# Optimization experiments

Measured on AMD Instinct MI355X. Metric: run time of the kernel, lower is better.

Reference implementation:

```python
import jax, jax.numpy as jnp
import numpy as np
from jax import lax

# dims
B, H, W, C = 32, 64, 64, 256
FEATURES, HEADS, NQ = 256, 8, 2
K, STRIDE, PAD = 3, 2, 1
HD = FEATURES // HEADS  # head dim = 32


def setup_inputs() -> dict:
    key = jax.random.key(0)
    ks = jax.random.split(key, 7)
    x = jax.random.normal(ks[0], (B, H, W, C), jnp.float32)
    # learned shared queries: truncated normal * sqrt(1/head_dim)
    query = jax.random.truncated_normal(ks[1], -2.0, 2.0, (NQ, FEATURES), jnp.float32) * np.float32(np.sqrt(1.0 / HD))
    Wk = jax.random.normal(ks[2], (C, FEATURES), jnp.float32) * np.float32(np.sqrt(1.0 / C))  # lecun
    Wv = jax.random.normal(ks[3], (C, FEATURES), jnp.float32) * np.float32(np.sqrt(1.0 / C))
    rpe_bias = jax.random.truncated_normal(ks[4], -2.0, 2.0, (K * K, NQ * HEADS), jnp.float32) * np.float32(0.02)
    attn_scale_w = jax.random.normal(ks[5], (K * K, NQ * HEADS), jnp.float32) * np.float32(0.02)
    Wo = jax.random.normal(ks[6], (FEATURES, FEATURES), jnp.float32) * np.float32(np.sqrt(1.0 / FEATURES))
    return {"x": x, "query": query, "Wk": Wk, "Wv": Wv,
            "rpe_bias": rpe_bias, "attn_scale_w": attn_scale_w, "Wo": Wo}


def _qna_forward(x, query, Wk, Wv, rpe_bias, attn_scale_w, Wo):
    # --- queries: reshape to [NQ, HEADS, HD], unit-normalize per head, depth-scale ---
    q = query.reshape(NQ, HEADS, HD)
    q = q / (jnp.linalg.norm(q, axis=-1, keepdims=True) + 1e-6)
    q = q / jnp.sqrt(HD).astype(q.dtype)

    # --- fused QK: (q Wk^T) applied to x, never materializing per-window keys ---
    Wk_r = Wk.reshape(C, HEADS, HD)
    qWk = jnp.einsum('qHd,DHd->DqH', q, Wk_r)              # [C, NQ, HEADS]
    cost = jnp.einsum('bijD,DqH->bijqH', x, qWk)            # [B, H, W, NQ, HEADS]
    cost_exp = jnp.exp(cost - lax.stop_gradient(jnp.max(cost)))  # global shift, cancels in softmax

    # --- values ---
    v = jnp.einsum('bijD,DF->bijF', x, Wv)                  # [B, H, W, FEATURES]
    v_cost_exp = cost_exp[..., None] * v.reshape(B, H, W, 1, HEADS, HD)
    v_cost_exp = v_cost_exp.reshape(B, H, W, NQ * FEATURES)

    # --- relative position bias + per-offset query mixing scale ---
    rpe = rpe_bias.reshape(K, K, 1, NQ * HEADS)
    rpe_exp = jnp.exp(rpe - lax.stop_gradient(jnp.max(rpe)))  # shift cancels (appears in num & den)
    scale = attn_scale_w.reshape(K, K, 1, NQ * HEADS)
    num_kernel = jnp.repeat(rpe_exp * scale, HD, axis=-1)   # [K, K, 1, NQ*FEATURES]

    # numerator: windowed sum of exp(cost)*v weighted by exp(rpe)*scale (depthwise conv)
    num = lax.conv_general_dilated(
        v_cost_exp, num_kernel, window_strides=(STRIDE, STRIDE),
        padding=((PAD, PAD), (PAD, PAD)), feature_group_count=NQ * FEATURES,
        dimension_numbers=('NHWC', 'HWIO', 'NHWC'))
    # denominator: windowed sum of exp(cost) weighted by exp(rpe)
    den = lax.conv_general_dilated(
        cost_exp.reshape(B, H, W, NQ * HEADS), rpe_exp, window_strides=(STRIDE, STRIDE),
        padding=((PAD, PAD), (PAD, PAD)), feature_group_count=NQ * HEADS,
        dimension_numbers=('NHWC', 'HWIO', 'NHWC'))
    ho, wo = num.shape[1], num.shape[2]

    out = num.reshape(B, ho, wo, NQ, HEADS, HD) / den.reshape(B, ho, wo, NQ, HEADS, 1)
    out = out.sum(axis=3).reshape(B, ho, wo, FEATURES)      # combine queries
    return jnp.einsum('bijF,FO->bijO', out, Wo)             # output projection


def reference(x, query, Wk, Wv, rpe_bias, attn_scale_w, Wo):
    return _qna_forward(x, query, Wk, Wv, rpe_bias, attn_scale_w, Wo)
```

## Files before the change

kernel.cpp:

```cpp
#include <hip/hip_runtime.h>
#include <math.h>

typedef __attribute__((ext_vector_type(8))) short bf16x8;
typedef __attribute__((ext_vector_type(4))) float floatx4;

static __device__ __forceinline__ short f2bf(float f) {
    union { float f; unsigned u; } a; a.f = f;
    unsigned r = a.u + 0x7fffu + ((a.u >> 16) & 1u);
    return (short)(r >> 16);
}
static __device__ __forceinline__ float bf2f(short s) {
    union { unsigned u; float f; } c; c.u = ((unsigned)(unsigned short)s) << 16;
    return c.f;
}

__global__ __launch_bounds__(256) void prep_kernel(
    const float* __restrict__ query,
    const float* __restrict__ Wk,
    const float* __restrict__ rpe_bias,
    const float* __restrict__ attn_scale_w,
    const float* __restrict__ Wv,
    const float* __restrict__ Wo,
    float* __restrict__ rpe_exp,
    float* __restrict__ rpe_scale,
    short* __restrict__ Bq,
    short* __restrict__ Wvh,
    short* __restrict__ Bo)
{
    __shared__ float qn[16 * 33];
    __shared__ float Wt[16][260];
    __shared__ float qwk_s[16][17];
    int tid = threadIdx.x, bb = blockIdx.x;

    for (int i = tid; i < 512; i += 256) {
        int qq  = i >> 8;
        int rem = i & 255;
        int h   = rem >> 5;
        int d   = rem & 31;
        qn[((qq << 3) + h) * 33 + d] = query[i];
    }
    for (int i = tid; i < 16 * 256; i += 256)
        Wt[i >> 8][i & 255] = Wk[bb * 16 * 256 + i];
    __syncthreads();
    if (tid < 16) {
        float s = 0.f;
        #pragma unroll
        for (int d = 0; d < 32; ++d) { float t = qn[tid * 33 + d]; s += t * t; }
        float inv = 1.0f / ((sqrtf(s) + 1e-6f) * sqrtf(32.0f));
        #pragma unroll
        for (int d = 0; d < 32; ++d) qn[tid * 33 + d] *= inv;
    }
    __syncthreads();

    int g  = tid & 15;
    int Dl = tid >> 4;
    int h2 = g & 7;
    float acc = 0.f;
    #pragma unroll
    for (int d = 0; d < 32; ++d)
        acc += qn[g * 33 + d] * Wt[Dl][h2 * 32 + d];
    qwk_s[Dl][g] = acc;
    __syncthreads();

    {
        int kl = tid >> 4, gg = tid & 15;
        int k  = bb * 16 + kl;
        int kc = k >> 5, q5 = k & 31, qd = q5 >> 3, j = q5 & 7;
        int lane = qd * 16 + gg;
        Bq[kc * 512 + lane * 8 + j] = f2bf(qwk_s[kl][gg]);
    }

    for (int kl = 0; kl < 16; ++kl) {
        int k  = bb * 16 + kl;
        int kc = k >> 5, q5 = k & 31, qd = q5 >> 3, j = q5 & 7;
        int n  = tid;
        int gg = n & 15;
        int lane = qd * 16 + gg;
        float vv = Wv[k * 256 + n];
        float vo = Wo[k * 256 + n];
        int nt  = n >> 4;
        Wvh[nt * 4096 + kc * 512 + lane * 8 + j] = f2bf(vv);
        Bo[nt * 4096 + kc * 512 + lane * 8 + j]  = f2bf(vo);
    }

    if (bb == 0 && tid < 144) {
        float r = expf(rpe_bias[tid]);
        rpe_exp[tid]   = r;
        rpe_scale[tid] = r * attn_scale_w[tid];
    }
}

#define XROWA 264
__global__ __launch_bounds__(256, 4) void va_kernel(
    const float* __restrict__ x,
    const short* __restrict__ Bq,
    const short* __restrict__ Wvh,
    short* __restrict__ V,
    float* __restrict__ cesg)
{
    __shared__ short XA[64 * XROWA];
    int tid  = threadIdx.x;
    int lane = tid & 63, wv = tid >> 6;
    int m16  = lane & 15, quad = lane >> 4;
    size_t p0 = (size_t)blockIdx.x * 64;

    #pragma unroll
    for (int i = 0; i < 8; ++i) {
        int it  = tid + i * 256;
        int row = it >> 5, l = it & 31;
        const float* xp = x + (p0 + row) * 256 + l * 8;
        float4 f0 = *(const float4*)xp;
        float4 f1 = *(const float4*)(xp + 4);
        bf16x8 s;
        s[0] = f2bf(f0.x); s[1] = f2bf(f0.y); s[2] = f2bf(f0.z); s[3] = f2bf(f0.w);
        s[4] = f2bf(f1.x); s[5] = f2bf(f1.y); s[6] = f2bf(f1.z); s[7] = f2bf(f1.w);
        *(bf16x8*)&XA[row * XROWA + l * 8] = s;
    }
    __syncthreads();

    {
        floatx4 acc = (floatx4){0.f, 0.f, 0.f, 0.f};
        const short* bq   = Bq + lane * 8;
        const short* xrow = &XA[(wv * 16 + m16) * XROWA + quad * 8];
        #pragma unroll
        for (int kc = 0; kc < 8; ++kc) {
            bf16x8 a = *(const bf16x8*)(xrow + kc * 32);
            acc = __builtin_amdgcn_mfma_f32_16x16x32_bf16(
                      a, *(const bf16x8*)(bq + kc * 512), acc, 0, 0, 0);
        }
        #pragma unroll
        for (int r = 0; r < 4; ++r)
            cesg[(p0 + wv * 16 + quad * 4 + r) * 16 + m16] = expf(acc[r]);
    }

    floatx4 acc[4][4];
    #pragma unroll
    for (int m = 0; m < 4; ++m)
        #pragma unroll
        for (int ln = 0; ln < 4; ++ln)
            acc[m][ln] = (floatx4){0.f, 0.f, 0.f, 0.f};

    const short* bvw = Wvh + (4 * wv) * 4096 + lane * 8;
    #pragma unroll
    for (int kc = 0; kc < 8; ++kc) {
        bf16x8 B0 = *(const bf16x8*)(bvw + 0 * 4096 + kc * 512);
        bf16x8 B1 = *(const bf16x8*)(bvw + 1 * 4096 + kc * 512);
        bf16x8 B2 = *(const bf16x8*)(bvw + 2 * 4096 + kc * 512);
        bf16x8 B3 = *(const bf16x8*)(bvw + 3 * 4096 + kc * 512);
        #pragma unroll
        for (int m = 0; m < 4; ++m) {
            bf16x8 a = *(const bf16x8*)&XA[(m * 16 + m16) * XROWA + kc * 32 + quad * 8];
            acc[m][0] = __builtin_amdgcn_mfma_f32_16x16x32_bf16(a, B0, acc[m][0], 0, 0, 0);
            acc[m][1] = __builtin_amdgcn_mfma_f32_16x16x32_bf16(a, B1, acc[m][1], 0, 0, 0);
            acc[m][2] = __builtin_amdgcn_mfma_f32_16x16x32_bf16(a, B2, acc[m][2], 0, 0, 0);
            acc[m][3] = __builtin_amdgcn_mfma_f32_16x16x32_bf16(a, B3, acc[m][3], 0, 0, 0);
        }
    }
    __syncthreads();

    #pragma unroll
    for (int m = 0; m < 4; ++m)
        #pragma unroll
        for (int ln = 0; ln < 4; ++ln)
            #pragma unroll
            for (int r = 0; r < 4; ++r)
                XA[(m * 16 + quad * 4 + r) * XROWA + (4 * wv + ln) * 16 + m16] =
                    f2bf(acc[m][ln][r]);
    __syncthreads();

    #pragma unroll
    for (int i = 0; i < 8; ++i) {
        int it  = tid + i * 256;
        int row = it >> 5, l = it & 31;
        *(bf16x8*)&V[(p0 + row) * 256 + l * 8] =
            *(const bf16x8*)&XA[row * XROWA + l * 8];
    }
}

#define OROW 264
__global__ __launch_bounds__(512) void qb_kernel(
    const float* __restrict__ cesg,
    const short* __restrict__ V,
    const float* __restrict__ rpe_exp,
    const float* __restrict__ rpe_scale,
    const short* __restrict__ Bo,
    float* __restrict__ out)
{
    __shared__ short out_tr[16 * OROW];
    __shared__ float wcoefs[8][9][16];
    __shared__ float invden[16][16];

    int tid  = threadIdx.x;
    int lane = tid & 63, wv = tid >> 6;
    int m16  = lane & 15, quad = lane >> 4;

    int blk0 = blockIdx.x;
    int blk  = ((blk0 & 7) << 8) | (blk0 >> 3);
    int b   = blk >> 6;
    int io  = (blk >> 1) & 31;
    int hf  = blk & 1;
    int i0  = io * 2 - 1;
    int jbase = hf * 32 - 1;

    if (tid < 256) {
        int op = tid >> 4, g = tid & 15;
        float den = 0.f;
        #pragma unroll
        for (int w = 0; w < 9; ++w) {
            int ky = w / 3, kx = w - ky * 3;
            int ii = i0 + ky, jj = jbase + 2 * op + kx;
            if ((unsigned)ii < 64u && (unsigned)jj < 64u) {
                size_t pix = ((size_t)((b << 6) + ii) << 6) + jj;
                den = fmaf(rpe_exp[w * 16 + g], cesg[pix * 16 + g], den);
            }
        }
        invden[op][g] = 1.0f / den;
    }
    __syncthreads();

    for (int it = tid; it < 1152; it += 512) {
        int op = it / 72, r = it - op * 72;
        int w = r >> 3, h = r & 7;
        int ky = w / 3, kx = w - ky * 3;
        int ii = i0 + ky, jj = jbase + 2 * op + kx;
        float v = 0.f;
        if ((unsigned)ii < 64u && (unsigned)jj < 64u) {
            size_t pix = ((size_t)((b << 6) + ii) << 6) + jj;
            v = cesg[pix * 16 + h]     * rpe_scale[w * 16 + h]     * invden[op][h] +
                cesg[pix * 16 + 8 + h] * rpe_scale[w * 16 + 8 + h] * invden[op][8 + h];
        }
        wcoefs[h][w][op] = v;
    }
    __syncthreads();

    {
        int op = tid >> 5;
        int nc = tid & 31;
        int h  = nc >> 2;
        float wcv[9];
        #pragma unroll
        for (int w = 0; w < 9; ++w) wcv[w] = wcoefs[h][w][op];

        float o[8];
        #pragma unroll
        for (int j = 0; j < 8; ++j) o[j] = 0.f;
        #pragma unroll
        for (int w = 0; w < 9; ++w) {
            int ky = w / 3, kx = w - ky * 3;
            int ii = i0 + ky, jj = jbase + 2 * op + kx;
            bool valid = ((unsigned)ii < 64u) && ((unsigned)jj < 64u);
            size_t pix = valid ? (((size_t)((b << 6) + ii) << 6) + jj) : 0;
            bf16x8 vv = *(const bf16x8*)&V[pix * 256 + nc * 8];
            #pragma unroll
            for (int j = 0; j < 8; ++j)
                o[j] = fmaf(wcv[w], bf2f(vv[j]), o[j]);
        }
        bf16x8 ob;
        #pragma unroll
        for (int j = 0; j < 8; ++j) ob[j] = f2bf(o[j]);
        *(bf16x8*)&out_tr[op * OROW + nc * 8] = ob;
    }
    __syncthreads();

    {
        floatx4 acc0 = (floatx4){0.f, 0.f, 0.f, 0.f};
        floatx4 acc1 = (floatx4){0.f, 0.f, 0.f, 0.f};
        int nt0 = wv * 2;
        const short* bp = Bo + nt0 * 4096 + lane * 8;
        #pragma unroll
        for (int kc = 0; kc < 8; ++kc) {
            bf16x8 a  = *(const bf16x8*)&out_tr[m16 * OROW + kc * 32 + quad * 8];
            bf16x8 b0 = *(const bf16x8*)(bp + kc * 512);
            bf16x8 b1 = *(const bf16x8*)(bp + 4096 + kc * 512);
            acc0 = __builtin_amdgcn_mfma_f32_16x16x32_bf16(a, b0, acc0, 0, 0, 0);
            acc1 = __builtin_amdgcn_mfma_f32_16x16x32_bf16(a, b1, acc1, 0, 0, 0);
        }
        size_t op0 = (size_t)blk * 16;
        #pragma unroll
        for (int r = 0; r < 4; ++r) {
            out[(op0 + quad * 4 + r) * 256 + nt0 * 16 + m16]       = acc0[r];
            out[(op0 + quad * 4 + r) * 256 + (nt0 + 1) * 16 + m16] = acc1[r];
        }
    }
}

extern "C" void kernel_launch(void* const* d_in, const int* in_sizes, int n_in,
                              void* d_out, int out_size, void* d_ws, size_t ws_size,
                              hipStream_t stream)
{
    const float* x     = (const float*)d_in[0];
    const float* query = (const float*)d_in[1];
    const float* Wk    = (const float*)d_in[2];
    const float* Wv    = (const float*)d_in[3];
    const float* rpe   = (const float*)d_in[4];
    const float* asw   = (const float*)d_in[5];
    const float* Wo    = (const float*)d_in[6];
    float* out = (float*)d_out;

    float* ws        = (float*)d_ws;
    float* rpe_exp   = ws;
    float* rpe_scale = ws + 144;
    short* Bq        = (short*)(ws + 288);
    short* Wvh       = (short*)(ws + 288 + 2048);
    short* Bo        = (short*)(ws + 288 + 2048 + 32768);
    short* V         = (short*)(ws + 68608);
    float* cesg      = ws + 68608 + 16777216;

    prep_kernel<<<dim3(16), dim3(256), 0, stream>>>(query, Wk, rpe, asw, Wv, Wo,
                                                    rpe_exp, rpe_scale, Bq, Wvh, Bo);
    va_kernel<<<dim3(2048), dim3(256), 0, stream>>>(x, Bq, Wvh, V, cesg);
    qb_kernel<<<dim3(2048), dim3(512), 0, stream>>>(cesg, V, rpe_exp, rpe_scale,
                                                    Bo, out);
}
```

Before: 272.0 us.

## Make va_kernel persistent with double-buffered x prefetch and direct V stores

Each va_kernel block now processes four 64-pixel tiles, prefetching the next tile of x into registers while running the MFMAs on the current tile from a double-buffered LDS array. The grid shrinks from 2048 to 512 blocks and launch bounds drop to 2 waves per SIMD. V is written straight from the accumulators as scattered 2-byte global stores, replacing the LDS transpose and coalesced 16-byte stores. The aim is to hide global load latency behind compute and save the transpose barriers, at the cost of more registers, lower occupancy, and uncoalesced V writes.

```diff
diff --git a/kernel.cpp b/kernel.cpp
--- a/kernel.cpp
+++ b/kernel.cpp
@@ -91,89 +91,122 @@
 }
 
 #define XROWA 264
-__global__ __launch_bounds__(256, 4) void va_kernel(
+__global__ __launch_bounds__(256, 2) void va_kernel(
     const float* __restrict__ x,
     const short* __restrict__ Bq,
     const short* __restrict__ Wvh,
     short* __restrict__ V,
     float* __restrict__ cesg)
 {
-    __shared__ short XA[64 * XROWA];
+    __shared__ short XA[2][64 * XROWA];
     int tid  = threadIdx.x;
     int lane = tid & 63, wv = tid >> 6;
     int m16  = lane & 15, quad = lane >> 4;
-    size_t p0 = (size_t)blockIdx.x * 64;
-
-    #pragma unroll
-    for (int i = 0; i < 8; ++i) {
-        int it  = tid + i * 256;
-        int row = it >> 5, l = it & 31;
-        const float* xp = x + (p0 + row) * 256 + l * 8;
-        float4 f0 = *(const float4*)xp;
-        float4 f1 = *(const float4*)(xp + 4);
-        bf16x8 s;
-        s[0] = f2bf(f0.x); s[1] = f2bf(f0.y); s[2] = f2bf(f0.z); s[3] = f2bf(f0.w);
-        s[4] = f2bf(f1.x); s[5] = f2bf(f1.y); s[6] = f2bf(f1.z); s[7] = f2bf(f1.w);
-        *(bf16x8*)&XA[row * XROWA + l * 8] = s;
-    }
-    __syncthreads();
+
+    float4 fA[8], fB[8];
 
     {
-        floatx4 acc = (floatx4){0.f, 0.f, 0.f, 0.f};
-        const short* bq   = Bq + lane * 8;
-        const short* xrow = &XA[(wv * 16 + m16) * XROWA + quad * 8];
+        size_t pb = (size_t)blockIdx.x * 64;
+        #pragma unroll
+        for (int i = 0; i < 8; ++i) {
+            int it = tid + i * 256, row = it >> 5, l = it & 31;
+            const float* xp = x + (pb + row) * 256 + l * 8;
+            fA[i] = *(const float4*)xp;
+            fB[i] = *(const float4*)(xp + 4);
+        }
+        #pragma unroll
+        for (int i = 0; i < 8; ++i) {
+            int it = tid + i * 256, row = it >> 5, l = it & 31;
+            bf16x8 s;
+            s[0] = f2bf(fA[i].x); s[1] = f2bf(fA[i].y);
+            s[2] = f2bf(fA[i].z); s[3] = f2bf(fA[i].w);
+            s[4] = f2bf(fB[i].x); s[5] = f2bf(fB[i].y);
+            s[6] = f2bf(fB[i].z); s[7] = f2bf(fB[i].w);
+            *(bf16x8*)&XA[0][row * XROWA + l * 8] = s;
+        }
+    }
+    __syncthreads();
+
+    const short* bvw = Wvh + (4 * wv) * 4096 + lane * 8;
+    const short* bq  = Bq + lane * 8;
+
+    for (int t = 0; t < 4; ++t) {
+        int cur = t & 1;
+        size_t p0 = (size_t)(blockIdx.x + t * 512) * 64;
+
+        if (t < 3) {
+            size_t pn = (size_t)(blockIdx.x + (t + 1) * 512) * 64;
+            #pragma unroll
+            for (int i = 0; i < 8; ++i) {
+                int it = tid + i * 256, row = it >> 5, l = it & 31;
+                const float* xp = x + (pn + row) * 256 + l * 8;
+                fA[i] = *(const float4*)xp;
+                fB[i] = *(const float4*)(xp + 4);
+            }
+        }
+
+        float ce[4];
+        {
+            floatx4 acq = (floatx4){0.f, 0.f, 0.f, 0.f};
+            const short* xrow = &XA[cur][(wv * 16 + m16) * XROWA + quad * 8];
+            #pragma unroll
+            for (int kc = 0; kc < 8; ++kc) {
+                bf16x8 a = *(const bf16x8*)(xrow + kc * 32);
+                acq = __builtin_amdgcn_mfma_f32_16x16x32_bf16(
+                          a, *(const bf16x8*)(bq + kc * 512), acq, 0, 0, 0);
+            }
+            #pragma unroll
+            for (int r = 0; r < 4; ++r) ce[r] = expf(acq[r]);
+        }
+
+        floatx4 acc[4][4];
+        #pragma unroll
+        for (int m = 0; m < 4; ++m)
+            #pragma unroll
+            for (int ln = 0; ln < 4; ++ln)
+                acc[m][ln] = (floatx4){0.f, 0.f, 0.f, 0.f};
         #pragma unroll
         for (int kc = 0; kc < 8; ++kc) {
-            bf16x8 a = *(const bf16x8*)(xrow + kc * 32);
-            acc = __builtin_amdgcn_mfma_f32_16x16x32_bf16(
-                      a, *(const bf16x8*)(bq + kc * 512), acc, 0, 0, 0);
-        }
+            bf16x8 B0 = *(const bf16x8*)(bvw + 0 * 4096 + kc * 512);
+            bf16x8 B1 = *(const bf16x8*)(bvw + 1 * 4096 + kc * 512);
+            bf16x8 B2 = *(const bf16x8*)(bvw + 2 * 4096 + kc * 512);
+            bf16x8 B3 = *(const bf16x8*)(bvw + 3 * 4096 + kc * 512);
+            #pragma unroll
+            for (int m = 0; m < 4; ++m) {
+                bf16x8 a = *(const bf16x8*)
+                    &XA[cur][(m * 16 + m16) * XROWA + kc * 32 + quad * 8];
+                acc[m][0] = __builtin_amdgcn_mfma_f32_16x16x32_bf16(a, B0, acc[m][0], 0, 0, 0);
+                acc[m][1] = __builtin_amdgcn_mfma_f32_16x16x32_bf16(a, B1, acc[m][1], 0, 0, 0);
+                acc[m][2] = __builtin_amdgcn_mfma_f32_16x16x32_bf16(a, B2, acc[m][2], 0, 0, 0);
+                acc[m][3] = __builtin_amdgcn_mfma_f32_16x16x32_bf16(a, B3, acc[m][3], 0, 0, 0);
+            }
+        }
+
+        if (t < 3) {
+            #pragma unroll
+            for (int i = 0; i < 8; ++i) {
+                int it = tid + i * 256, row = it >> 5, l = it & 31;
+                bf16x8 s;
+                s[0] = f2bf(fA[i].x); s[1] = f2bf(fA[i].y);
+                s[2] = f2bf(fA[i].z); s[3] = f2bf(fA[i].w);
+                s[4] = f2bf(fB[i].x); s[5] = f2bf(fB[i].y);
+                s[6] = f2bf(fB[i].z); s[7] = f2bf(fB[i].w);
+                *(bf16x8*)&XA[cur ^ 1][row * XROWA + l * 8] = s;
+            }
+        }
+        __syncthreads();
+
         #pragma unroll
         for (int r = 0; r < 4; ++r)
-            cesg[(p0 + wv * 16 + quad * 4 + r) * 16 + m16] = expf(acc[r]);
-    }
-
-    floatx4 acc[4][4];
-    #pragma unroll
-    for (int m = 0; m < 4; ++m)
-        #pragma unroll
-        for (int ln = 0; ln < 4; ++ln)
-            acc[m][ln] = (floatx4){0.f, 0.f, 0.f, 0.f};
-
-    const short* bvw = Wvh + (4 * wv) * 4096 + lane * 8;
-    #pragma unroll
-    for (int kc = 0; kc < 8; ++kc) {
-        bf16x8 B0 = *(const bf16x8*)(bvw + 0 * 4096 + kc * 512);
-        bf16x8 B1 = *(const bf16x8*)(bvw + 1 * 4096 + kc * 512);
-        bf16x8 B2 = *(const bf16x8*)(bvw + 2 * 4096 + kc * 512);
-        bf16x8 B3 = *(const bf16x8*)(bvw + 3 * 4096 + kc * 512);
-        #pragma unroll
-        for (int m = 0; m < 4; ++m) {
-            bf16x8 a = *(const bf16x8*)&XA[(m * 16 + m16) * XROWA + kc * 32 + quad * 8];
-            acc[m][0] = __builtin_amdgcn_mfma_f32_16x16x32_bf16(a, B0, acc[m][0], 0, 0, 0);
-            acc[m][1] = __builtin_amdgcn_mfma_f32_16x16x32_bf16(a, B1, acc[m][1], 0, 0, 0);
-            acc[m][2] = __builtin_amdgcn_mfma_f32_16x16x32_bf16(a, B2, acc[m][2], 0, 0, 0);
-            acc[m][3] = __builtin_amdgcn_mfma_f32_16x16x32_bf16(a, B3, acc[m][3], 0, 0, 0);
-        }
-    }
-    __syncthreads();
-
-    #pragma unroll
-    for (int m = 0; m < 4; ++m)
-        #pragma unroll
-        for (int ln = 0; ln < 4; ++ln)
-            #pragma unroll
-            for (int r = 0; r < 4; ++r)
-                XA[(m * 16 + quad * 4 + r) * XROWA + (4 * wv + ln) * 16 + m16] =
-                    f2bf(acc[m][ln][r]);
-    __syncthreads();
-
-    #pragma unroll
-    for (int i = 0; i < 8; ++i) {
-        int it  = tid + i * 256;
-        int row = it >> 5, l = it & 31;
-        *(bf16x8*)&V[(p0 + row) * 256 + l * 8] =
-            *(const bf16x8*)&XA[row * XROWA + l * 8];
+            cesg[(p0 + wv * 16 + quad * 4 + r) * 16 + m16] = ce[r];
+        #pragma unroll
+        for (int m = 0; m < 4; ++m)
+            #pragma unroll
+            for (int ln = 0; ln < 4; ++ln)
+                #pragma unroll
+                for (int r = 0; r < 4; ++r)
+                    V[(p0 + m * 16 + quad * 4 + r) * 256 +
+                      (4 * wv + ln) * 16 + m16] = f2bf(acc[m][ln][r]);
     }
 }
 
@@ -308,7 +341,7 @@
 
     prep_kernel<<<dim3(16), dim3(256), 0, stream>>>(query, Wk, rpe, asw, Wv, Wo,
                                                     rpe_exp, rpe_scale, Bq, Wvh, Bo);
-    va_kernel<<<dim3(2048), dim3(256), 0, stream>>>(x, Bq, Wvh, V, cesg);
+    va_kernel<<<dim3(512), dim3(256), 0, stream>>>(x, Bq, Wvh, V, cesg);
     qb_kernel<<<dim3(2048), dim3(512), 0, stream>>>(cesg, V, rpe_exp, rpe_scale,
                                                     Bo, out);
 }
```

New measurement: 306.6 us. +12.7%, slower.

## Fuse value projection and windowed attention into a single halo-tiled kernel

Applied to the files above, without the earlier changes.

Merges the two-stage pipeline into one kernel. Each block loads a 3x17-pixel input halo of x, computes exp(cost) and the value projection in shared memory, then does the windowed weighted sum and output projection for 8 output pixels. This removes the global round-trip of the bf16 V tensor and the exp-cost buffer, and one launch. In exchange, overlapping halos are re-read and the key/value matmuls are recomputed. The value GEMM is padded to 64 rows for 51 valid pixels, and the output GEMM wastes half its 16 rows.

```diff
diff --git a/kernel.cpp b/kernel.cpp
--- a/kernel.cpp
+++ b/kernel.cpp
@@ -90,47 +90,79 @@
     }
 }
 
-#define XROWA 264
-__global__ __launch_bounds__(256, 4) void va_kernel(
+#define XROW 264
+#define CESR 19
+__global__ __launch_bounds__(256, 4) void fused8_kernel(
     const float* __restrict__ x,
+    const float* __restrict__ rpe_exp,
+    const float* __restrict__ rpe_scale,
     const short* __restrict__ Bq,
     const short* __restrict__ Wvh,
-    short* __restrict__ V,
-    float* __restrict__ cesg)
+    const short* __restrict__ Bo,
+    float* __restrict__ out)
 {
-    __shared__ short XA[64 * XROWA];
+    __shared__ short XA[64 * XROW];
+    __shared__ __align__(16) unsigned char pool[4224];
+    __shared__ float wcoefs[8][9][8];
+    __shared__ float invden[8][16];
+
+    float* ces    = (float*)pool;
+    short* out_tr = (short*)pool;
+
     int tid  = threadIdx.x;
     int lane = tid & 63, wv = tid >> 6;
     int m16  = lane & 15, quad = lane >> 4;
-    size_t p0 = (size_t)blockIdx.x * 64;
+
+    int blk0 = blockIdx.x;
+    int blk  = ((blk0 & 7) << 9) | (blk0 >> 3);
+    int b   = blk >> 7;
+    int io  = (blk >> 2) & 31;
+    int oc  = blk & 3;
+    int i0  = io * 2 - 1;
+    int jbase = oc * 16 - 1;
 
     #pragma unroll
     for (int i = 0; i < 8; ++i) {
         int it  = tid + i * 256;
-        int row = it >> 5, l = it & 31;
-        const float* xp = x + (p0 + row) * 256 + l * 8;
-        float4 f0 = *(const float4*)xp;
-        float4 f1 = *(const float4*)(xp + 4);
+        int row = it >> 5;
+        int l   = it & 31;
+        int ky  = row / 17;
+        int jloc = row - ky * 17;
+        int ii = i0 + ky, jj = jbase + jloc;
+        bool valid = (row < 51) && ((unsigned)ii < 64u) && ((unsigned)jj < 64u);
         bf16x8 s;
-        s[0] = f2bf(f0.x); s[1] = f2bf(f0.y); s[2] = f2bf(f0.z); s[3] = f2bf(f0.w);
-        s[4] = f2bf(f1.x); s[5] = f2bf(f1.y); s[6] = f2bf(f1.z); s[7] = f2bf(f1.w);
-        *(bf16x8*)&XA[row * XROWA + l * 8] = s;
-    }
-    __syncthreads();
-
-    {
-        floatx4 acc = (floatx4){0.f, 0.f, 0.f, 0.f};
+        if (valid) {
+            const float* xp = x + ((size_t)(((b << 6) + ii) << 6) + jj) * 256 + l * 8;
+            float4 f0 = *(const float4*)xp;
+            float4 f1 = *(const float4*)(xp + 4);
+            s[0] = f2bf(f0.x); s[1] = f2bf(f0.y); s[2] = f2bf(f0.z); s[3] = f2bf(f0.w);
+            s[4] = f2bf(f1.x); s[5] = f2bf(f1.y); s[6] = f2bf(f1.z); s[7] = f2bf(f1.w);
+        } else {
+            #pragma unroll
+            for (int j = 0; j < 8; ++j) s[j] = 0;
+        }
+        *(bf16x8*)&XA[row * XROW + l * 8] = s;
+    }
+    __syncthreads();
+
+    {
+        floatx4 accc = (floatx4){0.f, 0.f, 0.f, 0.f};
         const short* bq   = Bq + lane * 8;
-        const short* xrow = &XA[(wv * 16 + m16) * XROWA + quad * 8];
+        const short* xrow = &XA[(wv * 16 + m16) * XROW + quad * 8];
         #pragma unroll
         for (int kc = 0; kc < 8; ++kc) {
             bf16x8 a = *(const bf16x8*)(xrow + kc * 32);
-            acc = __builtin_amdgcn_mfma_f32_16x16x32_bf16(
-                      a, *(const bf16x8*)(bq + kc * 512), acc, 0, 0, 0);
-        }
-        #pragma unroll
-        for (int r = 0; r < 4; ++r)
-            cesg[(p0 + wv * 16 + quad * 4 + r) * 16 + m16] = expf(acc[r]);
+            accc = __builtin_amdgcn_mfma_f32_16x16x32_bf16(
+                       a, *(const bf16x8*)(bq + kc * 512), accc, 0, 0, 0);
+        }
+        #pragma unroll
+        for (int r = 0; r < 4; ++r) {
+            int p = wv * 16 + quad * 4 + r;
+            int ky = p / 17, jloc = p - ky * 17;
+            int ii = i0 + ky, jj = jbase + jloc;
+            bool valid = (p < 51) && ((unsigned)ii < 64u) && ((unsigned)jj < 64u);
+            if (p < 51) ces[p * CESR + m16] = valid ? expf(accc[r]) : 0.f;
+        }
     }
 
     floatx4 acc[4][4];
@@ -139,21 +171,23 @@
         #pragma unroll
         for (int ln = 0; ln < 4; ++ln)
             acc[m][ln] = (floatx4){0.f, 0.f, 0.f, 0.f};
-
-    const short* bvw = Wvh + (4 * wv) * 4096 + lane * 8;
-    #pragma unroll
-    for (int kc = 0; kc < 8; ++kc) {
-        bf16x8 B0 = *(const bf16x8*)(bvw + 0 * 4096 + kc * 512);
-        bf16x8 B1 = *(const bf16x8*)(bvw + 1 * 4096 + kc * 512);
-        bf16x8 B2 = *(const bf16x8*)(bvw + 2 * 4096 + kc * 512);
-        bf16x8 B3 = *(const bf16x8*)(bvw + 3 * 4096 + kc * 512);
-        #pragma unroll
-        for (int m = 0; m < 4; ++m) {
-            bf16x8 a = *(const bf16x8*)&XA[(m * 16 + m16) * XROWA + kc * 32 + quad * 8];
-            acc[m][0] = __builtin_amdgcn_mfma_f32_16x16x32_bf16(a, B0, acc[m][0], 0, 0, 0);
-            acc[m][1] = __builtin_amdgcn_mfma_f32_16x16x32_bf16(a, B1, acc[m][1], 0, 0, 0);
-            acc[m][2] = __builtin_amdgcn_mfma_f32_16x16x32_bf16(a, B2, acc[m][2], 0, 0, 0);
-            acc[m][3] = __builtin_amdgcn_mfma_f32_16x16x32_bf16(a, B3, acc[m][3], 0, 0, 0);
+    {
+        const short* bvw = Wvh + (4 * wv) * 4096 + lane * 8;
+        #pragma unroll
+        for (int kc = 0; kc < 8; ++kc) {
+            bf16x8 B0 = *(const bf16x8*)(bvw + 0 * 4096 + kc * 512);
+            bf16x8 B1 = *(const bf16x8*)(bvw + 1 * 4096 + kc * 512);
+            bf16x8 B2 = *(const bf16x8*)(bvw + 2 * 4096 + kc * 512);
+            bf16x8 B3 = *(const bf16x8*)(bvw + 3 * 4096 + kc * 512);
+            #pragma unroll
+            for (int m = 0; m < 4; ++m) {
+                bf16x8 a = *(const bf16x8*)
+                    &XA[(m * 16 + m16) * XROW + kc * 32 + quad * 8];
+                acc[m][0] = __builtin_amdgcn_mfma_f32_16x16x32_bf16(a, B0, acc[m][0], 0, 0, 0);
+                acc[m][1] = __builtin_amdgcn_mfma_f32_16x16x32_bf16(a, B1, acc[m][1], 0, 0, 0);
+                acc[m][2] = __builtin_amdgcn_mfma_f32_16x16x32_bf16(a, B2, acc[m][2], 0, 0, 0);
+                acc[m][3] = __builtin_amdgcn_mfma_f32_16x16x32_bf16(a, B3, acc[m][3], 0, 0, 0);
+            }
         }
     }
     __syncthreads();
@@ -164,72 +198,31 @@
         for (int ln = 0; ln < 4; ++ln)
             #pragma unroll
             for (int r = 0; r < 4; ++r)
-                XA[(m * 16 + quad * 4 + r) * XROWA + (4 * wv + ln) * 16 + m16] =
+                XA[(m * 16 + quad * 4 + r) * XROW + (4 * wv + ln) * 16 + m16] =
                     f2bf(acc[m][ln][r]);
     __syncthreads();
 
-    #pragma unroll
-    for (int i = 0; i < 8; ++i) {
-        int it  = tid + i * 256;
-        int row = it >> 5, l = it & 31;
-        *(bf16x8*)&V[(p0 + row) * 256 + l * 8] =
-            *(const bf16x8*)&XA[row * XROWA + l * 8];
-    }
-}
-
-#define OROW 264
-__global__ __launch_bounds__(512) void qb_kernel(
-    const float* __restrict__ cesg,
-    const short* __restrict__ V,
-    const float* __restrict__ rpe_exp,
-    const float* __restrict__ rpe_scale,
-    const short* __restrict__ Bo,
-    float* __restrict__ out)
-{
-    __shared__ short out_tr[16 * OROW];
-    __shared__ float wcoefs[8][9][16];
-    __shared__ float invden[16][16];
-
-    int tid  = threadIdx.x;
-    int lane = tid & 63, wv = tid >> 6;
-    int m16  = lane & 15, quad = lane >> 4;
-
-    int blk0 = blockIdx.x;
-    int blk  = ((blk0 & 7) << 8) | (blk0 >> 3);
-    int b   = blk >> 6;
-    int io  = (blk >> 1) & 31;
-    int hf  = blk & 1;
-    int i0  = io * 2 - 1;
-    int jbase = hf * 32 - 1;
-
-    if (tid < 256) {
+    if (tid < 128) {
         int op = tid >> 4, g = tid & 15;
         float den = 0.f;
         #pragma unroll
         for (int w = 0; w < 9; ++w) {
             int ky = w / 3, kx = w - ky * 3;
-            int ii = i0 + ky, jj = jbase + 2 * op + kx;
-            if ((unsigned)ii < 64u && (unsigned)jj < 64u) {
-                size_t pix = ((size_t)((b << 6) + ii) << 6) + jj;
-                den = fmaf(rpe_exp[w * 16 + g], cesg[pix * 16 + g], den);
-            }
+            int row = ky * 17 + 2 * op + kx;
+            den = fmaf(rpe_exp[w * 16 + g], ces[row * CESR + g], den);
         }
         invden[op][g] = 1.0f / den;
     }
     __syncthreads();
 
-    for (int it = tid; it < 1152; it += 512) {
+    for (int it = tid; it < 576; it += 256) {
         int op = it / 72, r = it - op * 72;
         int w = r >> 3, h = r & 7;
         int ky = w / 3, kx = w - ky * 3;
-        int ii = i0 + ky, jj = jbase + 2 * op + kx;
-        float v = 0.f;
-        if ((unsigned)ii < 64u && (unsigned)jj < 64u) {
-            size_t pix = ((size_t)((b << 6) + ii) << 6) + jj;
-            v = cesg[pix * 16 + h]     * rpe_scale[w * 16 + h]     * invden[op][h] +
-                cesg[pix * 16 + 8 + h] * rpe_scale[w * 16 + 8 + h] * invden[op][8 + h];
-        }
-        wcoefs[h][w][op] = v;
+        int row = ky * 17 + 2 * op + kx;
+        wcoefs[h][w][op] =
+            ces[row * CESR + h]     * rpe_scale[w * 16 + h]     * invden[op][h] +
+            ces[row * CESR + 8 + h] * rpe_scale[w * 16 + 8 + h] * invden[op][8 + h];
     }
     __syncthreads();
 
@@ -247,10 +240,8 @@
         #pragma unroll
         for (int w = 0; w < 9; ++w) {
             int ky = w / 3, kx = w - ky * 3;
-            int ii = i0 + ky, jj = jbase + 2 * op + kx;
-            bool valid = ((unsigned)ii < 64u) && ((unsigned)jj < 64u);
-            size_t pix = valid ? (((size_t)((b << 6) + ii) << 6) + jj) : 0;
-            bf16x8 vv = *(const bf16x8*)&V[pix * 256 + nc * 8];
+            int row = ky * 17 + 2 * op + kx;
+            bf16x8 vv = *(const bf16x8*)&XA[row * XROW + nc * 8];
             #pragma unroll
             for (int j = 0; j < 8; ++j)
                 o[j] = fmaf(wcv[w], bf2f(vv[j]), o[j]);
@@ -258,28 +249,36 @@
         bf16x8 ob;
         #pragma unroll
         for (int j = 0; j < 8; ++j) ob[j] = f2bf(o[j]);
-        *(bf16x8*)&out_tr[op * OROW + nc * 8] = ob;
-    }
-    __syncthreads();
-
-    {
-        floatx4 acc0 = (floatx4){0.f, 0.f, 0.f, 0.f};
-        floatx4 acc1 = (floatx4){0.f, 0.f, 0.f, 0.f};
-        int nt0 = wv * 2;
-        const short* bp = Bo + nt0 * 4096 + lane * 8;
+        *(bf16x8*)&out_tr[op * XROW + nc * 8] = ob;
+    }
+    __syncthreads();
+
+    {
+        floatx4 a5[4];
+        #pragma unroll
+        for (int ln = 0; ln < 4; ++ln) a5[ln] = (floatx4){0.f, 0.f, 0.f, 0.f};
+        int mr = m16 & 7;
+        const short* bp = Bo + (4 * wv) * 4096 + lane * 8;
         #pragma unroll
         for (int kc = 0; kc < 8; ++kc) {
-            bf16x8 a  = *(const bf16x8*)&out_tr[m16 * OROW + kc * 32 + quad * 8];
-            bf16x8 b0 = *(const bf16x8*)(bp + kc * 512);
-            bf16x8 b1 = *(const bf16x8*)(bp + 4096 + kc * 512);
-            acc0 = __builtin_amdgcn_mfma_f32_16x16x32_bf16(a, b0, acc0, 0, 0, 0);
-            acc1 = __builtin_amdgcn_mfma_f32_16x16x32_bf16(a, b1, acc1, 0, 0, 0);
-        }
-        size_t op0 = (size_t)blk * 16;
-        #pragma unroll
-        for (int r = 0; r < 4; ++r) {
-            out[(op0 + quad * 4 + r) * 256 + nt0 * 16 + m16]       = acc0[r];
-            out[(op0 + quad * 4 + r) * 256 + (nt0 + 1) * 16 + m16] = acc1[r];
+            bf16x8 a  = *(const bf16x8*)&out_tr[mr * XROW + kc * 32 + quad * 8];
+            a5[0] = __builtin_amdgcn_mfma_f32_16x16x32_bf16(
+                        a, *(const bf16x8*)(bp + 0 * 4096 + kc * 512), a5[0], 0, 0, 0);
+            a5[1] = __builtin_amdgcn_mfma_f32_16x16x32_bf16(
+                        a, *(const bf16x8*)(bp + 1 * 4096 + kc * 512), a5[1], 0, 0, 0);
+            a5[2] = __builtin_amdgcn_mfma_f32_16x16x32_bf16(
+                        a, *(const bf16x8*)(bp + 2 * 4096 + kc * 512), a5[2], 0, 0, 0);
+            a5[3] = __builtin_amdgcn_mfma_f32_16x16x32_bf16(
+                        a, *(const bf16x8*)(bp + 3 * 4096 + kc * 512), a5[3], 0, 0, 0);
+        }
+        if (quad < 2) {
+            size_t op0 = (size_t)blk * 8;
+            #pragma unroll
+            for (int ln = 0; ln < 4; ++ln)
+                #pragma unroll
+                for (int r = 0; r < 4; ++r)
+                    out[(op0 + quad * 4 + r) * 256 + (4 * wv + ln) * 16 + m16] =
+                        a5[ln][r];
         }
     }
 }
@@ -303,12 +302,9 @@
     short* Bq        = (short*)(ws + 288);
     short* Wvh       = (short*)(ws + 288 + 2048);
     short* Bo        = (short*)(ws + 288 + 2048 + 32768);
-    short* V         = (short*)(ws + 68608);
-    float* cesg      = ws + 68608 + 16777216;
 
     prep_kernel<<<dim3(16), dim3(256), 0, stream>>>(query, Wk, rpe, asw, Wv, Wo,
                                                     rpe_exp, rpe_scale, Bq, Wvh, Bo);
-    va_kernel<<<dim3(2048), dim3(256), 0, stream>>>(x, Bq, Wvh, V, cesg);
-    qb_kernel<<<dim3(2048), dim3(512), 0, stream>>>(cesg, V, rpe_exp, rpe_scale,
-                                                    Bo, out);
-}
+    fused8_kernel<<<dim3(4096), dim3(256), 0, stream>>>(x, rpe_exp, rpe_scale,
+                                                        Bq, Wvh, Bo, out);
+}
```

After: 268.2 us. About the same (-1.4%).
